# Kernel tuning notes

Measured on AMD Instinct MI355X. Metric: run time of the kernel, lower is better.

The kernel has to match this reference:

```python
import jax, jax.numpy as jnp
import numpy as np

B, N, D, H = 2, 512, 384, 12
SQK, SV, PQ, PV = 16, 16, 4, 8
SCALE = 1.0 / np.sqrt(SQK + 4 * PQ)  # attention_scale, point_pair_dim=4
EPS = 1e-12


def setup_inputs() -> dict:
    key = jax.random.key(0)
    ks = jax.random.split(key, 10)

    def w(k, fan_in, fan_out):
        return (jax.random.normal(k, (fan_in, fan_out), jnp.float32) / np.sqrt(fan_in))

    return {
        "hidden": jax.random.normal(ks[0], (B, N, D), jnp.float32),
        "xyz": jax.random.normal(ks[1], (B, N, 3), jnp.float32),
        "W_qk": w(ks[2], D, 2 * H * SQK), "b_qk": jnp.zeros((2 * H * SQK,), jnp.float32),
        "W_vs": w(ks[3], D, H * SV), "b_vs": jnp.zeros((H * SV,), jnp.float32),
        "W_so": w(ks[4], H * SV, D), "b_so": jnp.zeros((D,), jnp.float32),
        "W_pqk": w(ks[5], D, H * PQ * 3), "b_pqk": jnp.zeros((H * PQ * 3,), jnp.float32),
        "W_pv": w(ks[6], D, H * PV * 3), "b_pv": jnp.zeros((H * PV * 3,), jnp.float32),
        "W_po": w(ks[7], H * PV * 3, D), "b_po": jnp.zeros((D,), jnp.float32),
        "W_fp": w(ks[8], 2 * D, D), "b_fp": jnp.zeros((D,), jnp.float32),
    }


def reference(hidden, xyz, W_qk, b_qk, W_vs, b_vs, W_so, b_so,
              W_pqk, b_pqk, W_pv, b_pv, W_po, b_po, W_fp, b_fp):
    # scalar q/k/v (note: heads are NOT split in the attention matmuls, per source)
    qk = hidden @ W_qk + b_qk                       # [B,N,2*H*SQK]
    q_s, k_s = jnp.split(qk, 2, axis=-1)            # [B,N,H*SQK] each
    v_s = hidden @ W_vs + b_vs                      # [B,N,H*SV]

    # points; k_points = q_points in source
    qp = (hidden @ W_pqk + b_pqk).reshape(B, N, H, PQ, 3)
    vp = hidden @ W_pv + b_pv                       # [B,N,H*PV*3]

    scalar_attn = jnp.einsum('bid,bjd->bij', q_s, k_s)  # [B,N,N]

    # fused pairwise point features: dist(q_i, k_j) + sum of 3 cosine components
    # = dist + cos_sim, per (head, point); avoid materializing [B,N,N,H,P,3].
    dot = jnp.einsum('bihpc,bjhpc->bijhp', qp, qp)      # [B,N,N,H,PQ]
    n2 = jnp.sum(qp * qp, axis=-1)                      # [B,N,H,PQ]
    d2 = n2[:, :, None] + n2[:, None] - 2.0 * dot
    dist = jnp.sqrt(jnp.maximum(d2, 0.0) + EPS)
    nrm = jnp.sqrt(n2 + EPS)
    cos = dot / (nrm[:, :, None] * nrm[:, None])
    point_attn = jnp.sum(dist + cos, axis=(-1, -2))     # [B,N,N]

    attn = jax.nn.softmax((scalar_attn + point_attn) * SCALE, axis=-1)

    scalar_result = jnp.einsum('bij,bjd->bid', attn, v_s)   # [B,N,H*SV]
    point_result = jnp.einsum('bij,bjd->bid', attn, vp)     # [B,N,H*PV*3]

    scalar_result = scalar_result @ W_so + b_so             # [B,N,D]
    point_result = point_result @ W_po + b_po               # [B,N,D]

    result = jnp.concatenate([scalar_result, point_result], axis=-1) @ W_fp + b_fp
    delta_xyz = point_result.reshape(B, N, -1, 3).mean(axis=2)  # [B,N,3]
    return result, xyz + delta_xyz
```

## Files before the change

kernel.cpp:

```cpp
#include <hip/hip_runtime.h>
#include <math.h>

typedef unsigned short u16;
typedef __attribute__((ext_vector_type(8))) short bf16x8;
typedef __attribute__((ext_vector_type(4))) float f32x4;

#define BB 2
#define NN 512
#define SCALEF 0.17677669529663687f

__device__ __forceinline__ u16 f2bf(float x) {
  union { float f; unsigned u; } c; c.f = x;
  unsigned r = (c.u + 0x7FFFu + ((c.u >> 16) & 1u)) >> 16;
  return (u16)r;
}
__device__ __forceinline__ float bf2f(u16 h) {
  union { unsigned u; float f; } c; c.u = ((unsigned)h) << 16;
  return c.f;
}
__device__ __forceinline__ void pack8(const float* v, bf16x8& h, bf16x8& l) {
#pragma unroll
  for (int j = 0; j < 8; ++j) {
    u16 hi = f2bf(v[j]);
    h[j] = (short)hi;
    l[j] = (short)f2bf(v[j] - bf2f(hi));
  }
}
#define MFMA3(ACC, AH, AL, BH, BL)                                              \
  ACC = __builtin_amdgcn_mfma_f32_16x16x32_bf16(AH, BH, ACC, 0, 0, 0);          \
  ACC = __builtin_amdgcn_mfma_f32_16x16x32_bf16(AH, BL, ACC, 0, 0, 0);          \
  ACC = __builtin_amdgcn_mfma_f32_16x16x32_bf16(AL, BH, ACC, 0, 0, 0);

template<int MR, int NF>
__device__ __forceinline__ void mfma_tile(
    const u16* __restrict__ Ah, const u16* __restrict__ Al, int lda,
    const u16* __restrict__ Bh, const u16* __restrict__ Bl, int ldb,
    int kBeg, int kEnd, int arow, int bcol, f32x4 (&acc)[MR][NF]) {
  const int lane = threadIdx.x & 63;
  const int rr = lane & 15, kg = lane >> 4;
  const u16* pah = Ah + (size_t)(arow + rr) * lda + kg * 8;
  const u16* pal = Al + (size_t)(arow + rr) * lda + kg * 8;
  const u16* pbh = Bh + (size_t)(bcol + rr) * ldb + kg * 8;
  const u16* pbl = Bl + (size_t)(bcol + rr) * ldb + kg * 8;
#pragma unroll 2
  for (int k0 = kBeg; k0 < kEnd; k0 += 32) {
    bf16x8 a_h[MR], a_l[MR], b_h[NF], b_l[NF];
#pragma unroll
    for (int m = 0; m < MR; ++m) {
      a_h[m] = *(const bf16x8*)(pah + (size_t)m * 16 * lda + k0);
      a_l[m] = *(const bf16x8*)(pal + (size_t)m * 16 * lda + k0);
    }
#pragma unroll
    for (int f = 0; f < NF; ++f) {
      b_h[f] = *(const bf16x8*)(pbh + (size_t)f * 16 * ldb + k0);
      b_l[f] = *(const bf16x8*)(pbl + (size_t)f * 16 * ldb + k0);
    }
#pragma unroll
    for (int m = 0; m < MR; ++m)
#pragma unroll
      for (int f = 0; f < NF; ++f) { MFMA3(acc[m][f], a_h[m], a_l[m], b_h[f], b_l[f]) }
  }
}

__global__ __launch_bounds__(512) void k_input(
    const float* __restrict__ hidden,
    const float* __restrict__ W_qk, const float* __restrict__ b_qk,
    const float* __restrict__ W_vs, const float* __restrict__ b_vs,
    const float* __restrict__ W_pv, const float* __restrict__ b_pv,
    const float* __restrict__ W_pqk, const float* __restrict__ b_pqk,
    const float* __restrict__ W_so, const float* __restrict__ b_so,
    const float* __restrict__ W_po, const float* __restrict__ b_po,
    const float* __restrict__ W_fp, const float* __restrict__ b_fp,
    u16* __restrict__ QKh, u16* __restrict__ QKl,
    u16* __restrict__ VRh, u16* __restrict__ VRl,
    float* __restrict__ QPf,
    u16* __restrict__ WCTh, u16* __restrict__ WCTl,
    float* __restrict__ bc, float* __restrict__ Wdf) {
  const int tid = threadIdx.x;
  if (blockIdx.x >= 21) {
    const int cx = blockIdx.x - 21, ky = blockIdx.y;
    if (ky < 10) {
      const int w = tid >> 6, lane = tid & 63;
      if (w >= 3) return;
      const int rr = lane & 15, kg = lane >> 4;
      const int c0 = cx * 48;
      const int kbase = ky * 48 + w * 16;
      const float* Wop; int moff;
      if (kbase < 192) { Wop = W_so + (size_t)kbase * 384; moff = 0; }
      else             { Wop = W_po + (size_t)(kbase - 192) * 384; moff = 384; }
      f32x4 acc[3] = {};
      const float* pa = Wop + (size_t)rr * 384 + kg * 8;
      const float* pw = W_fp + (size_t)moff * 384 + c0 + rr;
      for (int m0 = 0; m0 < 384; m0 += 32) {
        bf16x8 a_h, a_l, b_h[3], b_l[3];
        float v[8];
        *(float4*)&v[0] = *(const float4*)(pa + m0);
        *(float4*)&v[4] = *(const float4*)(pa + m0 + 4);
        pack8(v, a_h, a_l);
        const float* bp0 = pw + (size_t)(m0 + kg * 8) * 384;
#pragma unroll
        for (int f = 0; f < 3; ++f) {
          float u[8];
#pragma unroll
          for (int j = 0; j < 8; ++j) u[j] = bp0[(size_t)j * 384 + f * 16];
          pack8(u, b_h[f], b_l[f]);
        }
#pragma unroll
        for (int f = 0; f < 3; ++f) { MFMA3(acc[f], a_h, a_l, b_h[f], b_l[f]) }
      }
      const int rb = (lane >> 4) << 2, cc = lane & 15;
#pragma unroll
      for (int f = 0; f < 3; ++f) {
        int c = c0 + f * 16 + cc;
#pragma unroll
        for (int r = 0; r < 4; ++r) {
          int k = kbase + rb + r;
          float vv = acc[f][r];
          u16 hi = f2bf(vv);
          WCTh[(size_t)c * 480 + k] = hi;
          WCTl[(size_t)c * 480 + k] = f2bf(vv - bf2f(hi));
        }
      }
      return;
    }
    if (ky == 10) {
      const int colL = tid >> 3, part = tid & 7;
      if (colL >= 48) return;
      const int col = cx * 48 + colL;
      const float* bv = (part < 4) ? b_so : b_po;
      const int m0 = (part & 3) * 96;
      const float* wrow = W_fp + (size_t)part * 96 * 384 + col;
      float s0 = 0.f, s1 = 0.f, s2 = 0.f, s3 = 0.f;
#pragma unroll
      for (int i = 0; i < 96; i += 4) {
        s0 += bv[m0 + i]     * wrow[(size_t)(i)     * 384];
        s1 += bv[m0 + i + 1] * wrow[(size_t)(i + 1) * 384];
        s2 += bv[m0 + i + 2] * wrow[(size_t)(i + 2) * 384];
        s3 += bv[m0 + i + 3] * wrow[(size_t)(i + 3) * 384];
      }
      float s = (s0 + s1) + (s2 + s3);
      s += __shfl_down(s, 4, 8);
      s += __shfl_down(s, 2, 8);
      s += __shfl_down(s, 1, 8);
      if (part == 0) bc[col] = s + b_fp[col];
      return;
    }
    if (ky == 11) {
      const int out = tid >> 2, part = tid & 3;
      if (out < 108) {
        const int j = cx * 36 + out / 3, c = out - (out / 3) * 3;
        const float* src = W_po + (size_t)j * 384 + c + (size_t)part * 96;
        float s0 = 0.f, s1 = 0.f;
#pragma unroll
        for (int kk = 0; kk < 32; kk += 2) {
          s0 += src[3 * kk];
          s1 += src[3 * kk + 3];
        }
        float s = s0 + s1;
        s += __shfl_down(s, 2, 4);
        s += __shfl_down(s, 1, 4);
        if (part == 0) Wdf[j * 3 + c] = s * (1.0f / 128.f);
      } else if (cx == 0 && tid >= 432 && tid < 480) {
        int g = tid - 432, c = g >> 4, k0 = g & 15;
        float s = 0.f;
#pragma unroll
        for (int kk = 0; kk < 8; ++kk) s += b_po[3 * (k0 * 8 + kk) + c];
        for (int d = 8; d; d >>= 1) s += __shfl_down(s, d, 16);
        if (k0 == 0) Wdf[864 + c] = s * (1.0f / 128.f);
      }
      return;
    }
    return;
  }

  __shared__ f32x4 CB[7][2][3][64];
  const int w = tid >> 6, lane = tid & 63;
  const int rr = lane & 15, kg = lane >> 4;
  const int row0 = blockIdx.y * 32, col0 = blockIdx.x * 48;

  const float* W; const float* bias; int Ns, region;
  if (col0 < 384)      { W = W_qk;  Ns = 384; bias = b_qk + col0;          W += col0;       region = 0; }
  else if (col0 < 576) { W = W_vs;  Ns = 192; bias = b_vs + (col0 - 384);  W += col0 - 384; region = 1; }
  else if (col0 < 864) { W = W_pv;  Ns = 288; bias = b_pv + (col0 - 576);  W += col0 - 576; region = 1; }
  else                 { W = W_pqk; Ns = 144; bias = b_pqk + (col0 - 864); W += col0 - 864; region = 2; }

  f32x4 acc[2][3] = {};
  const float* pa = hidden + (size_t)(row0 + rr) * 384 + kg * 8;
  const float* pw = W + rr;
  for (int k0 = w * 32; k0 < 384; k0 += 256) {
    bf16x8 a_h[2], a_l[2], b_h[3], b_l[3];
#pragma unroll
    for (int m = 0; m < 2; ++m) {
      float v[8];
      *(float4*)&v[0] = *(const float4*)(pa + (size_t)m * 16 * 384 + k0);
      *(float4*)&v[4] = *(const float4*)(pa + (size_t)m * 16 * 384 + k0 + 4);
      pack8(v, a_h[m], a_l[m]);
    }
    const float* bp0 = pw + (size_t)(k0 + kg * 8) * Ns;
#pragma unroll
    for (int f = 0; f < 3; ++f) {
      float v[8];
#pragma unroll
      for (int j = 0; j < 8; ++j) v[j] = bp0[(size_t)j * Ns + f * 16];
      pack8(v, b_h[f], b_l[f]);
    }
#pragma unroll
    for (int m = 0; m < 2; ++m)
#pragma unroll
      for (int f = 0; f < 3; ++f) { MFMA3(acc[m][f], a_h[m], a_l[m], b_h[f], b_l[f]) }
  }
  if (w) {
#pragma unroll
    for (int m = 0; m < 2; ++m)
#pragma unroll
      for (int f = 0; f < 3; ++f) CB[w - 1][m][f][lane] = acc[m][f];
  }
  __syncthreads();
  if (w) return;
#pragma unroll
  for (int wv = 0; wv < 7; ++wv)
#pragma unroll
    for (int m = 0; m < 2; ++m)
#pragma unroll
      for (int f = 0; f < 3; ++f) acc[m][f] += CB[wv][m][f][lane];

  const int rb = (lane >> 4) << 2, cc = lane & 15;
  if (region == 0) {
#pragma unroll
    for (int f = 0; f < 3; ++f) {
      int n = col0 + f * 16 + cc;
      float bv = bias[f * 16 + cc];
#pragma unroll
      for (int m = 0; m < 2; ++m)
#pragma unroll
        for (int r = 0; r < 4; ++r) {
          float v = acc[m][f][r] + bv;
          int row = row0 + m * 16 + rb + r;
          u16 hi = f2bf(v);
          QKh[(size_t)row * 384 + n] = hi;
          QKl[(size_t)row * 384 + n] = f2bf(v - bf2f(hi));
        }
    }
  } else if (region == 2) {
#pragma unroll
    for (int f = 0; f < 3; ++f) {
      int c = (col0 - 864) + f * 16 + cc;
      float bv = bias[f * 16 + cc];
#pragma unroll
      for (int m = 0; m < 2; ++m)
#pragma unroll
        for (int r = 0; r < 4; ++r)
          QPf[(size_t)(row0 + m * 16 + rb + r) * 144 + c] = acc[m][f][r] + bv;
    }
  } else {
#pragma unroll
    for (int f = 0; f < 3; ++f) {
      int c = (col0 - 384) + f * 16 + cc;
      float bv = bias[f * 16 + cc];
#pragma unroll
      for (int m = 0; m < 2; ++m)
#pragma unroll
        for (int r = 0; r < 4; ++r) {
          float v = acc[m][f][r] + bv;
          int row = row0 + m * 16 + rb + r;
          u16 hi = f2bf(v);
          VRh[(size_t)row * 480 + c] = hi;
          VRl[(size_t)row * 480 + c] = f2bf(v - bf2f(hi));
        }
    }
  }
}

__global__ __launch_bounds__(512) void k_attn(
    const u16* __restrict__ QKh, const u16* __restrict__ QKl,
    const float* __restrict__ QPf,
    const u16* __restrict__ VRh, const u16* __restrict__ VRl,
    const u16* __restrict__ WCTh, const u16* __restrict__ WCTl,
    const float* __restrict__ Wdf,
    float* __restrict__ ATTf, u16* __restrict__ VCTh, u16* __restrict__ VCTl,
    float* __restrict__ VCdT) {
  __shared__ __align__(16) char smem[70912];
  const int tid = threadIdx.x;
  const int b = blockIdx.z;
  if (blockIdx.x >= 136) {
    const int xx = blockIdx.x - 136;
    if (xx < 256) {
      f32x4 (*CB)[3][64] = (f32x4 (*)[3][64])smem;
      u16 (*Dh)[16] = (u16 (*)[16])(smem + 21504);
      u16 (*Dl)[16] = (u16 (*)[16])(smem + 23040);
      const int tile = xx >> 3, cx = xx & 7;
      const int row0 = tile * 16, c0 = cx * 48;
      const int w = tid >> 6, lane = tid & 63;
      const int rr = lane & 15, kg = lane >> 4;
      const u16* pah = VRh + (size_t)(b * NN + row0 + rr) * 480 + kg * 8;
      const u16* pal = VRl + (size_t)(b * NN + row0 + rr) * 480 + kg * 8;
      const u16* pbh = WCTh + (size_t)(c0 + rr) * 480 + kg * 8;
      const u16* pbl = WCTl + (size_t)(c0 + rr) * 480 + kg * 8;
      f32x4 acc[3] = {};
      for (int k0 = w * 32; k0 < 480; k0 += 256) {
        bf16x8 a_h, a_l, b_h[3], b_l[3];
        a_h = *(const bf16x8*)(pah + k0);
        a_l = *(const bf16x8*)(pal + k0);
#pragma unroll
        for (int f = 0; f < 3; ++f) {
          b_h[f] = *(const bf16x8*)(pbh + (size_t)f * 16 * 480 + k0);
          b_l[f] = *(const bf16x8*)(pbl + (size_t)f * 16 * 480 + k0);
        }
#pragma unroll
        for (int f = 0; f < 3; ++f) { MFMA3(acc[f], a_h, a_l, b_h[f], b_l[f]) }
      }
      if (w) {
#pragma unroll
        for (int f = 0; f < 3; ++f) CB[w - 1][f][lane] = acc[f];
      }
      __syncthreads();
      if (w) return;
#pragma unroll
      for (int wv = 0; wv < 7; ++wv)
#pragma unroll
        for (int f = 0; f < 3; ++f) acc[f] += CB[wv][f][lane];
      const int rb = (lane >> 4) << 2, cc = lane & 15;
#pragma unroll
      for (int f = 0; f < 3; ++f)
#pragma unroll
        for (int r = 0; r < 4; ++r) {
          float v = acc[f][r];
          u16 hi = f2bf(v);
          Dh[f * 16 + cc][rb + r] = hi;
          Dl[f * 16 + cc][rb + r] = f2bf(v - bf2f(hi));
        }
      for (int u = lane; u < 192; u += 64) {
        int col = u >> 2, rem = u & 3, hl = rem >> 1, chunk = rem & 1;
        const u16* src = (hl ? Dl : Dh)[col] + chunk * 8;
        u16* dst = (hl ? VCTl : VCTh) + ((size_t)b * 384 + c0 + col) * 512 + row0 + chunk * 8;
        *(uint4*)dst = *(const uint4*)src;
      }
      return;
    }
    const int c = xx - 256;
    float* WdL = (float*)smem;
    for (int i = tid; i < 288; i += 512) WdL[i] = Wdf[i * 3 + c];
    __syncthreads();
    const u16* vh = VRh + (size_t)(b * NN + tid) * 480 + 192;
    const u16* vl = VRl + (size_t)(b * NN + tid) * 480 + 192;
    float s0 = 0.f, s1 = 0.f;
#pragma unroll 4
    for (int j = 0; j < 288; j += 2) {
      s0 += (bf2f(vh[j]) + bf2f(vl[j])) * WdL[j];
      s1 += (bf2f(vh[j + 1]) + bf2f(vl[j + 1])) * WdL[j + 1];
    }
    VCdT[((size_t)b * 3 + c) * 512 + tid] = s0 + s1;
    return;
  }
  float (*Pi)[244] = (float (*)[244])smem;
  float (*Pj)[244] = (float (*)[244])(smem + 31232);
  float* Sf = (float*)(smem + 62464);
  int t = blockIdx.x, ti_ = 0;
  while (t >= 16 - ti_) { t -= 16 - ti_; ++ti_; }
  const int tj_ = ti_ + t;
  const int i0 = ti_ * 32, j0 = tj_ * 32;
  const bool offdiag = (tj_ != ti_);
  for (int u = tid; u < 3072; u += 512) {
    int side = (u >= 1536) ? 1 : 0;
    int rem = u - side * 1536;
    int row = rem / 48, hp = rem - row * 48;
    int grow = b * NN + (side ? j0 : i0) + row;
    const float* p = QPf + (size_t)grow * 144 + hp * 3;
    float x = p[0], y = p[1], z = p[2];
    float n2 = x * x + y * y + z * z;
    float inv = __frsqrt_rn(n2 + 1e-12f);
    float* dst = side ? &Pj[row][0] : &Pi[row][0];
    ((float4*)dst)[hp] = make_float4(x, y, z, n2);
    dst[192 + hp] = inv;
  }
  __syncthreads();
  const int h = tid >> 8;
  const int t8 = tid & 255;
  const int tj = t8 & 15, ti = t8 >> 4;
  {
    float a00 = 0.f, a01 = 0.f, a10 = 0.f, a11 = 0.f;
    const float4* A0 = (const float4*)&Pi[ti][0];
    const float4* A1 = (const float4*)&Pi[ti + 16][0];
    const float4* B0 = (const float4*)&Pj[tj][0];
    const float4* B1 = (const float4*)&Pj[tj + 16][0];
    const float* iA0 = &Pi[ti][192];
    const float* iA1 = &Pi[ti + 16][192];
    const float* iB0 = &Pj[tj][192];
    const float* iB1 = &Pj[tj + 16][192];
    const int hpB = h * 24, hpE = hpB + 24;
#pragma unroll 4
    for (int hp = hpB; hp < hpE; ++hp) {
      float4 p0 = A0[hp], p1 = A1[hp], q0 = B0[hp], q1 = B1[hp];
      float va0 = iA0[hp], va1 = iA1[hp], vb0 = iB0[hp], vb1 = iB1[hp];
      {
        float dot = p0.x * q0.x + p0.y * q0.y + p0.z * q0.z;
        float d2 = fmaxf(fmaf(-2.f, dot, p0.w + q0.w), 0.f) + 1e-12f;
        a00 += d2 * __frsqrt_rn(d2) + dot * (va0 * vb0);
      }
      {
        float dot = p0.x * q1.x + p0.y * q1.y + p0.z * q1.z;
        float d2 = fmaxf(fmaf(-2.f, dot, p0.w + q1.w), 0.f) + 1e-12f;
        a01 += d2 * __frsqrt_rn(d2) + dot * (va0 * vb1);
      }
      {
        float dot = p1.x * q0.x + p1.y * q0.y + p1.z * q0.z;
        float d2 = fmaxf(fmaf(-2.f, dot, p1.w + q0.w), 0.f) + 1e-12f;
        a10 += d2 * __frsqrt_rn(d2) + dot * (va1 * vb0);
      }
      {
        float dot = p1.x * q1.x + p1.y * q1.y + p1.z * q1.z;
        float d2 = fmaxf(fmaf(-2.f, dot, p1.w + q1.w), 0.f) + 1e-12f;
        a11 += d2 * __frsqrt_rn(d2) + dot * (va1 * vb1);
      }
    }
    Sf[h * 1056 + ti * 33 + tj] = a00;
    Sf[h * 1056 + ti * 33 + tj + 16] = a01;
    Sf[h * 1056 + (ti + 16) * 33 + tj] = a10;
    Sf[h * 1056 + (ti + 16) * 33 + tj + 16] = a11;
  }
  const int w = tid >> 6, lane = tid & 63;
  const int dir = w >> 2, sub = w & 3;
  f32x4 q[1][1] = {};
  if (dir == 0) {
    int arow = b * NN + i0 + (sub >> 1) * 16;
    int brow = b * NN + j0 + (sub & 1) * 16;
    mfma_tile<1, 1>(QKh, QKl, 384, QKh + 192, QKl + 192, 384, 0, 192, arow, brow, q);
  } else if (offdiag) {
    int arow = b * NN + j0 + (sub >> 1) * 16;
    int brow = b * NN + i0 + (sub & 1) * 16;
    mfma_tile<1, 1>(QKh, QKl, 384, QKh + 192, QKl + 192, 384, 0, 192, arow, brow, q);
  }
  __syncthreads();
  const int rl = (sub >> 1) * 16 + ((lane >> 4) << 2);
  const int cl = (sub & 1) * 16 + (lane & 15);
  float* Cb = ATTf + (size_t)b * NN * NN;
  if (dir == 0) {
#pragma unroll
    for (int r = 0; r < 4; ++r)
      Cb[(size_t)(i0 + rl + r) * NN + j0 + cl] =
          q[0][0][r] + Sf[(rl + r) * 33 + cl] + Sf[1056 + (rl + r) * 33 + cl];
  } else if (offdiag) {
#pragma unroll
    for (int r = 0; r < 4; ++r)
      Cb[(size_t)(j0 + rl + r) * NN + i0 + cl] =
          q[0][0][r] + Sf[cl * 33 + rl + r] + Sf[1056 + cl * 33 + rl + r];
  }
}

__global__ __launch_bounds__(512) void k_pv_out(
    const float* __restrict__ ATTf,
    const u16* __restrict__ VCTh, const u16* __restrict__ VCTl,
    const float* __restrict__ VCdT, const float* __restrict__ bc,
    const float* __restrict__ Wdf, const float* __restrict__ xyz,
    float* __restrict__ out_res, float* __restrict__ out_xyz) {
  const int tid = threadIdx.x;
  const int b = blockIdx.z;
  const int row0 = blockIdx.y * 16;
  if (blockIdx.x == 8) {
    const int part = tid & 7, rest = tid >> 3;
    const int c = rest % 3, lt = rest / 3;
    if (lt < 16) {
      const float* arow = ATTf + ((size_t)b * NN + row0 + lt) * NN + part * 64;
      const float* vcd = VCdT + ((size_t)b * 3 + c) * 512 + part * 64;
      float s = 0.f, rs = 0.f;
#pragma unroll 8
      for (int kk = 0; kk < 64; ++kk) {
        float e = __expf(arow[kk] * SCALEF);
        s += e * vcd[kk];
        rs += e;
      }
#pragma unroll
      for (int d = 4; d; d >>= 1) { s += __shfl_down(s, d, 8); rs += __shfl_down(rs, d, 8); }
      if (part == 0) {
        size_t idx = ((size_t)b * NN + row0 + lt) * 3 + c;
        out_xyz[idx] = xyz[idx] + s / rs + Wdf[864 + c];
      }
    }
    return;
  }
  __shared__ f32x4 CB[7][3][64];
  __shared__ float RS[7][64];
  const int w = tid >> 6, lane = tid & 63;
  const int rr = lane & 15, kg = lane >> 4;
  const int col0 = blockIdx.x * 48;
  const float* pa = ATTf + (size_t)(b * NN + row0 + rr) * NN + kg * 8;
  const u16* pbh = VCTh + ((size_t)b * 384 + col0 + rr) * 512 + kg * 8;
  const u16* pbl = VCTl + ((size_t)b * 384 + col0 + rr) * 512 + kg * 8;
  f32x4 acc[3] = {};
  float rs = 0.f;
  for (int k0 = w * 32; k0 < NN; k0 += 256) {
    bf16x8 a_h, a_l, b_h[3], b_l[3];
    {
      float v[8];
      *(float4*)&v[0] = *(const float4*)(pa + k0);
      *(float4*)&v[4] = *(const float4*)(pa + k0 + 4);
#pragma unroll
      for (int j = 0; j < 8; ++j) { float e = __expf(v[j] * SCALEF); rs += e; v[j] = e; }
      pack8(v, a_h, a_l);
    }
#pragma unroll
    for (int f = 0; f < 3; ++f) {
      b_h[f] = *(const bf16x8*)(pbh + (size_t)f * 16 * 512 + k0);
      b_l[f] = *(const bf16x8*)(pbl + (size_t)f * 16 * 512 + k0);
    }
#pragma unroll
    for (int f = 0; f < 3; ++f) { MFMA3(acc[f], a_h, a_l, b_h[f], b_l[f]) }
  }
  if (w) {
#pragma unroll
    for (int f = 0; f < 3; ++f) CB[w - 1][f][lane] = acc[f];
    RS[w - 1][lane] = rs;
  }
  __syncthreads();
  if (w) return;
#pragma unroll
  for (int wv = 0; wv < 7; ++wv) {
#pragma unroll
    for (int f = 0; f < 3; ++f) acc[f] += CB[wv][f][lane];
    rs += RS[wv][lane];
  }
  rs += __shfl_xor(rs, 16);
  rs += __shfl_xor(rs, 32);
  const int rb = (lane >> 4) << 2, cc = lane & 15;
  float inv[4];
#pragma unroll
  for (int r = 0; r < 4; ++r) inv[r] = 1.0f / __shfl(rs, rb + r);
#pragma unroll
  for (int f = 0; f < 3; ++f) {
    int n = col0 + f * 16 + cc;
    float bcv = bc[n];
#pragma unroll
    for (int r = 0; r < 4; ++r)
      out_res[((size_t)b * NN + row0 + rb + r) * 384 + n] = acc[f][r] * inv[r] + bcv;
  }
}

extern "C" void kernel_launch(void* const* d_in, const int* in_sizes, int n_in,
                              void* d_out, int out_size, void* d_ws, size_t ws_size,
                              hipStream_t stream) {
  const float* hidden = (const float*)d_in[0];
  const float* xyz   = (const float*)d_in[1];
  const float* W_qk  = (const float*)d_in[2];
  const float* b_qk  = (const float*)d_in[3];
  const float* W_vs  = (const float*)d_in[4];
  const float* b_vs  = (const float*)d_in[5];
  const float* W_so  = (const float*)d_in[6];
  const float* b_so  = (const float*)d_in[7];
  const float* W_pqk = (const float*)d_in[8];
  const float* b_pqk = (const float*)d_in[9];
  const float* W_pv  = (const float*)d_in[10];
  const float* b_pv  = (const float*)d_in[11];
  const float* W_po  = (const float*)d_in[12];
  const float* b_po  = (const float*)d_in[13];
  const float* W_fp  = (const float*)d_in[14];
  const float* b_fp  = (const float*)d_in[15];

  float* out_res = (float*)d_out;
  float* out_xyz = out_res + (size_t)BB * NN * 384;

  u16* p   = (u16*)d_ws;
  u16* QKh  = p;           p += 393216;
  u16* QKl  = p;           p += 393216;
  u16* VRh  = p;           p += 491520;
  u16* VRl  = p;           p += 491520;
  u16* VCTh = p;           p += 393216;
  u16* VCTl = p;           p += 393216;
  u16* WCTh = p;           p += 184320;
  u16* WCTl = p;           p += 184320;
  float* QPf  = (float*)p; p += 2 * 147456;
  float* ATTf = (float*)p; p += 2 * 524288;
  float* VCdT = (float*)p; p += 2 * 3072;
  float* bcf  = (float*)p; p += 2 * 384;
  float* Wdf  = (float*)p;

  k_input<<<dim3(29, 32), 512, 0, stream>>>(hidden,
                                            W_qk, b_qk, W_vs, b_vs, W_pv, b_pv, W_pqk, b_pqk,
                                            W_so, b_so, W_po, b_po, W_fp, b_fp,
                                            QKh, QKl, VRh, VRl, QPf, WCTh, WCTl, bcf, Wdf);
  k_attn<<<dim3(395, 1, 2), 512, 0, stream>>>(QKh, QKl, QPf, VRh, VRl,
                                              WCTh, WCTl, Wdf,
                                              ATTf, VCTh, VCTl, VCdT);
  k_pv_out<<<dim3(9, 32, 2), 512, 0, stream>>>(ATTf, VCTh, VCTl, VCdT, bcf, Wdf, xyz,
                                               out_res, out_xyz);
}
```

Measured before the change: 72.70 us.

## Enlarge VC side-GEMM tiles to 32x96 and cut split-K depth

The auxiliary V×W GEMM blocks inside k_attn now each compute a 32-row by 96-column tile instead of 16x48. The 8 waves split into 2 column halves times 4 K-partitions rather than 8 K-partitions, with a reduction through shared memory and a cooperative write-out. This quarters the number of side blocks (grid 395→203) and reuses the A and B fragments across more MFMAs, reducing redundant global loads and reduction overhead. The trade-off is fewer blocks to spread across CUs, more registers per wave and an extra barrier.

```diff
diff --git a/kernel.cpp b/kernel.cpp
--- a/kernel.cpp
+++ b/kernel.cpp
@@ -284,60 +284,76 @@
   const int b = blockIdx.z;
   if (blockIdx.x >= 136) {
     const int xx = blockIdx.x - 136;
-    if (xx < 256) {
-      f32x4 (*CB)[3][64] = (f32x4 (*)[3][64])smem;
-      u16 (*Dh)[16] = (u16 (*)[16])(smem + 21504);
-      u16 (*Dl)[16] = (u16 (*)[16])(smem + 23040);
-      const int tile = xx >> 3, cx = xx & 7;
-      const int row0 = tile * 16, c0 = cx * 48;
+    if (xx < 64) {
+      f32x4 (*CB)[2][3][64] = (f32x4 (*)[2][3][64])smem;
+      u16 (*Dh)[32] = (u16 (*)[32])(smem + 36864);
+      u16 (*Dl)[32] = (u16 (*)[32])(smem + 43008);
+      const int tile = xx & 15, cg = xx >> 4;
+      const int row0 = tile * 32, c0 = cg * 96;
       const int w = tid >> 6, lane = tid & 63;
+      const int h2 = w & 1, p = w >> 1;
       const int rr = lane & 15, kg = lane >> 4;
       const u16* pah = VRh + (size_t)(b * NN + row0 + rr) * 480 + kg * 8;
       const u16* pal = VRl + (size_t)(b * NN + row0 + rr) * 480 + kg * 8;
-      const u16* pbh = WCTh + (size_t)(c0 + rr) * 480 + kg * 8;
-      const u16* pbl = WCTl + (size_t)(c0 + rr) * 480 + kg * 8;
-      f32x4 acc[3] = {};
-      for (int k0 = w * 32; k0 < 480; k0 += 256) {
-        bf16x8 a_h, a_l, b_h[3], b_l[3];
-        a_h = *(const bf16x8*)(pah + k0);
-        a_l = *(const bf16x8*)(pal + k0);
+      const u16* pbh = WCTh + (size_t)(c0 + h2 * 48 + rr) * 480 + kg * 8;
+      const u16* pbl = WCTl + (size_t)(c0 + h2 * 48 + rr) * 480 + kg * 8;
+      f32x4 acc[2][3] = {};
+      for (int k0 = p * 32; k0 < 480; k0 += 128) {
+        bf16x8 a_h[2], a_l[2], b_h[3], b_l[3];
+#pragma unroll
+        for (int m = 0; m < 2; ++m) {
+          a_h[m] = *(const bf16x8*)(pah + (size_t)m * 16 * 480 + k0);
+          a_l[m] = *(const bf16x8*)(pal + (size_t)m * 16 * 480 + k0);
+        }
 #pragma unroll
         for (int f = 0; f < 3; ++f) {
           b_h[f] = *(const bf16x8*)(pbh + (size_t)f * 16 * 480 + k0);
           b_l[f] = *(const bf16x8*)(pbl + (size_t)f * 16 * 480 + k0);
         }
 #pragma unroll
-        for (int f = 0; f < 3; ++f) { MFMA3(acc[f], a_h, a_l, b_h[f], b_l[f]) }
-      }
-      if (w) {
-#pragma unroll
-        for (int f = 0; f < 3; ++f) CB[w - 1][f][lane] = acc[f];
+        for (int m = 0; m < 2; ++m)
+#pragma unroll
+          for (int f = 0; f < 3; ++f) { MFMA3(acc[m][f], a_h[m], a_l[m], b_h[f], b_l[f]) }
+      }
+      if (p) {
+#pragma unroll
+        for (int m = 0; m < 2; ++m)
+#pragma unroll
+          for (int f = 0; f < 3; ++f) CB[h2 * 3 + p - 1][m][f][lane] = acc[m][f];
       }
       __syncthreads();
-      if (w) return;
-#pragma unroll
-      for (int wv = 0; wv < 7; ++wv)
-#pragma unroll
-        for (int f = 0; f < 3; ++f) acc[f] += CB[wv][f][lane];
-      const int rb = (lane >> 4) << 2, cc = lane & 15;
-#pragma unroll
-      for (int f = 0; f < 3; ++f)
-#pragma unroll
-        for (int r = 0; r < 4; ++r) {
-          float v = acc[f][r];
-          u16 hi = f2bf(v);
-          Dh[f * 16 + cc][rb + r] = hi;
-          Dl[f * 16 + cc][rb + r] = f2bf(v - bf2f(hi));
-        }
-      for (int u = lane; u < 192; u += 64) {
-        int col = u >> 2, rem = u & 3, hl = rem >> 1, chunk = rem & 1;
-        const u16* src = (hl ? Dl : Dh)[col] + chunk * 8;
-        u16* dst = (hl ? VCTl : VCTh) + ((size_t)b * 384 + c0 + col) * 512 + row0 + chunk * 8;
+      if (p == 0) {
+#pragma unroll
+        for (int part = 0; part < 3; ++part)
+#pragma unroll
+          for (int m = 0; m < 2; ++m)
+#pragma unroll
+            for (int f = 0; f < 3; ++f) acc[m][f] += CB[h2 * 3 + part][m][f][lane];
+        const int rb = (lane >> 4) << 2, cc = lane & 15;
+#pragma unroll
+        for (int m = 0; m < 2; ++m)
+#pragma unroll
+          for (int f = 0; f < 3; ++f)
+#pragma unroll
+            for (int r = 0; r < 4; ++r) {
+              float v = acc[m][f][r];
+              u16 hi = f2bf(v);
+              Dh[h2 * 48 + f * 16 + cc][m * 16 + rb + r] = hi;
+              Dl[h2 * 48 + f * 16 + cc][m * 16 + rb + r] = f2bf(v - bf2f(hi));
+            }
+      }
+      __syncthreads();
+      for (int u = tid; u < 768; u += 512) {
+        int buf = u >= 384;
+        int v2 = u - buf * 384;
+        int col = v2 >> 2, seg = v2 & 3;
+        const u16* src = (buf ? Dl[col] : Dh[col]) + seg * 8;
+        u16* dst = (buf ? VCTl : VCTh) + ((size_t)b * 384 + c0 + col) * 512 + row0 + seg * 8;
         *(uint4*)dst = *(const uint4*)src;
       }
       return;
     }
-    const int c = xx - 256;
+    const int c = xx - 64;
     float* WdL = (float*)smem;
     for (int i = tid; i < 288; i += 512) WdL[i] = Wdf[i * 3 + c];
     __syncthreads();
@@ -577,7 +593,7 @@
                                             W_qk, b_qk, W_vs, b_vs, W_pv, b_pv, W_pqk, b_pqk,
                                             W_so, b_so, W_po, b_po, W_fp, b_fp,
                                             QKh, QKl, VRh, VRl, QPf, WCTh, WCTl, bcf, Wdf);
-  k_attn<<<dim3(395, 1, 2), 512, 0, stream>>>(QKh, QKl, QPf, VRh, VRl,
+  k_attn<<<dim3(203, 1, 2), 512, 0, stream>>>(QKh, QKl, QPf, VRh, VRl,
                                               WCTh, WCTl, Wdf,
                                               ATTf, VCTh, VCTl, VCdT);
   k_pv_out<<<dim3(9, 32, 2), 512, 0, stream>>>(ATTf, VCTh, VCTl, VCdT, bcf, Wdf, xyz,
```

New measurement: 75.02 us. 1.03x slower.
